# Performance work log

Hardware: AMD Instinct MI355X
Metric: run time of the kernel (lower is better)

Reference implementation:

```python
import jax, jax.numpy as jnp
import numpy as np

NODE_SIZE = 50000
REL_SIZE = 2000
TRIPLE_SIZE = 1000000
HID = 128
DEPTH = 2


def _rows_covering(key, n_rows, n_seg):
    # sorted row indices guaranteeing every segment appears at least once
    extra = jax.random.randint(key, (n_rows - n_seg,), 0, n_seg)
    return jnp.sort(jnp.concatenate([jnp.arange(n_seg), extra])).astype(jnp.int32)


def setup_inputs() -> dict:
    key = jax.random.key(0)
    ks = jax.random.split(key, 12)
    adj = jnp.stack([_rows_covering(ks[0], TRIPLE_SIZE, NODE_SIZE),
                     jax.random.randint(ks[1], (TRIPLE_SIZE,), 0, NODE_SIZE, dtype=jnp.int32)])
    r_index = jnp.stack([jnp.arange(TRIPLE_SIZE, dtype=jnp.int32),
                         jax.random.randint(ks[2], (TRIPLE_SIZE,), 0, REL_SIZE, dtype=jnp.int32)])
    r_val = jax.random.uniform(ks[3], (TRIPLE_SIZE,), dtype=jnp.float32)
    ent_adj = jnp.stack([_rows_covering(ks[4], TRIPLE_SIZE, NODE_SIZE),
                         jax.random.randint(ks[5], (TRIPLE_SIZE,), 0, NODE_SIZE, dtype=jnp.int32)])
    rel_adj = jnp.stack([_rows_covering(ks[6], TRIPLE_SIZE, NODE_SIZE),
                         jax.random.randint(ks[7], (TRIPLE_SIZE,), 0, REL_SIZE, dtype=jnp.int32)])
    ent_emb = jax.random.normal(ks[8], (NODE_SIZE, HID), dtype=jnp.float32) * 0.05
    rel_emb = jax.random.normal(ks[9], (REL_SIZE, HID), dtype=jnp.float32) * 0.05
    attn_e = jax.random.normal(ks[10], (DEPTH, HID, 1), dtype=jnp.float32) * 0.1
    attn_r = jax.random.normal(ks[11], (DEPTH, HID, 1), dtype=jnp.float32) * 0.1
    return {"ent_emb": ent_emb, "rel_emb": rel_emb, "attn_e": attn_e, "attn_r": attn_r,
            "adj": adj, "r_index": r_index, "r_val": r_val,
            "ent_adj": ent_adj, "rel_adj": rel_adj}


def _avg(adj, emb, node_size):
    # sparse softmax over all-ones values == mean over neighbors
    rows, cols = adj[0], adj[1]
    deg = jax.ops.segment_sum(jnp.ones_like(rows, dtype=emb.dtype), rows, node_size)
    s = jax.ops.segment_sum(emb[cols], rows, node_size)  # [node_size, d]
    return s / jnp.maximum(deg, 1.0)[:, None]


def _segment_softmax(vals, seg, num_seg):
    m = jax.ops.segment_max(vals, seg, num_seg)
    e = jnp.exp(vals - m[seg])
    s = jax.ops.segment_sum(e, seg, num_seg)
    return e / s[seg]


def _nr_graph_attention(features, rel_emb, adj, r_index, r_val, attn_kernels):
    feats = jnp.tanh(features)
    outs = [feats]
    src, dst = adj[0], adj[1]
    for l in range(DEPTH):
        # sparse [T, R] @ rel_emb -> per-triple relation vector
        tri_rel = jax.ops.segment_sum(r_val[:, None] * rel_emb[r_index[1]], r_index[0], TRIPLE_SIZE)
        tri_rel = tri_rel / jnp.maximum(jnp.linalg.norm(tri_rel, axis=1, keepdims=True), 1e-12)
        neighs = feats[dst]  # [T, H]
        # Householder reflection of neighbor feature about tri_rel
        neighs = neighs - 2.0 * jnp.sum(neighs * tri_rel, axis=1, keepdims=True) * tri_rel
        att = jnp.squeeze(tri_rel @ attn_kernels[l], axis=-1)  # [T]
        a = _segment_softmax(att, src, NODE_SIZE)
        feats = jnp.tanh(jax.ops.segment_sum(neighs * a[:, None], src, NODE_SIZE))
        outs.append(feats)
    return jnp.concatenate(outs, axis=-1)  # [N, H*(DEPTH+1)]


def reference(ent_emb, rel_emb, attn_e, attn_r, adj, r_index, r_val, ent_adj, rel_adj):
    ent_feature = _avg(ent_adj, ent_emb, NODE_SIZE)  # [N, H]
    rel_feature = _avg(rel_adj, rel_emb, NODE_SIZE)  # [N, H]
    out_rel = _nr_graph_attention(rel_feature, rel_emb, adj, r_index, r_val, attn_r)
    out_ent = _nr_graph_attention(ent_feature, rel_emb, adj, r_index, r_val, attn_e)
    return jnp.concatenate([out_ent, out_rel], axis=-1)  # dropout rate 0 -> identity
```

## Files before the change

### kernel.cpp

```cpp
#include <hip/hip_runtime.h>
#include <hip/hip_fp16.h>
#include <math.h>

#define NN 50000
#define NR 2000
#define NT 1000000
#define HID 128
#define OSTRIDE 768
#define CH 256

typedef float f32x4 __attribute__((ext_vector_type(4)));
typedef unsigned u32x4 __attribute__((ext_vector_type(4)));
typedef unsigned u32x2 __attribute__((ext_vector_type(2)));
typedef _Float16 h16x2 __attribute__((ext_vector_type(2)));
typedef _Float16 h16x8 __attribute__((ext_vector_type(8)));

union U4H8 { u32x4 u; h16x8 h; };

__device__ __forceinline__ float wsum64(float v) {
#pragma unroll
  for (int off = 32; off > 0; off >>= 1) v += __shfl_xor(v, off, 64);
  return v;
}
__device__ __forceinline__ unsigned pack2(float x, float y) {
  __half2 h = __floats2half2_rn(x, y);
  union { __half2 h; unsigned u; } c; c.h = h; return c.u;
}
__device__ __forceinline__ float2 unpack2(unsigned u) {
  union { unsigned u; __half2 h; } c; c.u = u;
  return __half22float2(c.h);
}
__device__ __forceinline__ void nt_store4(const float4& v, float* p) {
  f32x4 t = {v.x, v.y, v.z, v.w};
  __builtin_nontemporal_store(t, (f32x4*)p);
}

__global__ void rowptr3_kernel(const int* __restrict__ a0, int* __restrict__ r0,
                               const int* __restrict__ a1, int* __restrict__ r1,
                               const int* __restrict__ a2, int* __restrict__ r2) {
  const int* rows = (blockIdx.y == 0) ? a0 : (blockIdx.y == 1) ? a1 : a2;
  int* rp = (blockIdx.y == 0) ? r0 : (blockIdx.y == 1) ? r1 : r2;
  int i = blockIdx.x * blockDim.x + threadIdx.x;
  int stride = gridDim.x * blockDim.x;
  for (int t = i; t < NT; t += stride) {
    if (t == 0 || rows[t] != rows[t - 1]) rp[rows[t]] = t;
  }
  if (i == 0) rp[NN] = NT;
}

__global__ __launch_bounds__(256) void relpre_kernel(
    const float* __restrict__ rel_emb, const float* __restrict__ attn_e,
    const float* __restrict__ attn_r, float4* __restrict__ e4,
    float* __restrict__ n2i_arr) {
  int wid = (blockIdx.x * blockDim.x + threadIdx.x) >> 6;
  int lane = threadIdx.x & 63;
  if (wid >= NR) return;
  const float2* e2 = (const float2*)rel_emb;
  float2 e = e2[(size_t)wid * 64 + lane];
  float p = wsum64(e.x * e.x + e.y * e.y);
  float inv_n = rsqrtf(p);
  const float* ks[4] = {attn_e, attn_e + HID, attn_r, attn_r + HID};
  float d[4];
#pragma unroll
  for (int j = 0; j < 4; ++j) {
    float2 a = ((const float2*)ks[j])[lane];
    d[j] = wsum64(e.x * a.x + e.y * a.y);
  }
  if (lane == 0) {
    e4[wid] = make_float4(expf(d[0] * inv_n), expf(d[1] * inv_n),
                          expf(d[2] * inv_n), expf(d[3] * inv_n));
    n2i_arr[wid] = 1.f / p;
  }
}

__global__ __launch_bounds__(256) void cvt_kernel(const float* __restrict__ ent,
                                                  const float* __restrict__ rel,
                                                  __half* __restrict__ enth,
                                                  __half* __restrict__ relh) {
  int i = blockIdx.x * blockDim.x + threadIdx.x;
  const int entu = NN * 16;
  const float4* s4;
  u32x4* d;
  int j;
  if (i < entu) {
    s4 = (const float4*)ent; d = (u32x4*)enth; j = i;
  } else {
    j = i - entu;
    if (j >= NR * 16) return;
    s4 = (const float4*)rel; d = (u32x4*)relh;
  }
  float4 a = s4[2 * j], b = s4[2 * j + 1];
  u32x4 w;
  w.x = pack2(a.x, a.y); w.y = pack2(a.z, a.w);
  w.z = pack2(b.x, b.y); w.w = pack2(b.z, b.w);
  __builtin_nontemporal_store(w, d + j);
}

__global__ __launch_bounds__(256) void wpre2_kernel(
    const int* __restrict__ rp, const int* __restrict__ dst,
    const int* __restrict__ rel_id, const float* __restrict__ r_val,
    const float4* __restrict__ e4, const float* __restrict__ n2i_arr,
    unsigned* __restrict__ pk, u32x2* __restrict__ wq0,
    u32x2* __restrict__ wq1) {
  int wid = (blockIdx.x * blockDim.x + threadIdx.x) >> 6;
  int lane = threadIdx.x & 63;
  if (wid >= NN) return;
  int t0 = rp[wid], t1 = rp[wid + 1];
  float4 s = make_float4(0.f, 0.f, 0.f, 0.f);
  for (int t = t0 + lane; t < t1; t += 64) {
    int r = rel_id[t];
    float rv = r_val[t];
    float4 ex = e4[r];
    if (rv <= 0.f) ex = make_float4(1.f, 1.f, 1.f, 1.f);
    s.x += ex.x; s.y += ex.y; s.z += ex.z; s.w += ex.w;
  }
  s.x = wsum64(s.x); s.y = wsum64(s.y); s.z = wsum64(s.z); s.w = wsum64(s.w);
  float4 inv = make_float4(1.f / s.x, 1.f / s.y, 1.f / s.z, 1.f / s.w);
  for (int t = t0 + lane; t < t1; t += 64) {
    int r = rel_id[t];
    float rv = r_val[t];
    int dn = dst[t];
    float4 ex = e4[r];
    float zi = n2i_arr[r];
    if (rv <= 0.f) { ex = make_float4(1.f, 1.f, 1.f, 1.f); zi = 0.f; }
    float we0 = ex.x * inv.x, wr0 = ex.z * inv.z;
    float we1 = ex.y * inv.y, wr1 = ex.w * inv.w;
    __builtin_nontemporal_store((unsigned)dn | ((unsigned)r << 16), pk + t);
    u32x2 a, b;
    a.x = pack2(we0, wr0); a.y = pack2(-2.f * we0 * zi, -2.f * wr0 * zi);
    b.x = pack2(we1, wr1); b.y = pack2(-2.f * we1 * zi, -2.f * wr1 * zi);
    __builtin_nontemporal_store(a, wq0 + t);
    __builtin_nontemporal_store(b, wq1 + t);
  }
}

__global__ __launch_bounds__(256) void avg_tanh_kernel(
    const int* __restrict__ rp_ent, const int* __restrict__ cols_ent,
    const int* __restrict__ rp_rel, const int* __restrict__ cols_rel,
    const __half* __restrict__ enth, const __half* __restrict__ relh,
    float* __restrict__ out, __half* __restrict__ c0h) {
  int wid = (blockIdx.x * blockDim.x + threadIdx.x) >> 6;
  int lane = threadIdx.x & 63;
  if (wid >= NN) return;
  int br = (wid >= NN / 2) ? 1 : 0;
  int pair = wid - br * (NN / 2);
  int node = pair * 2 + (lane >> 5);
  int sl = lane & 31;
  const int* rp = br ? rp_rel : rp_ent;
  const int* cols = br ? cols_rel : cols_ent;
  const u32x2* eb = (const u32x2*)(br ? relh : enth);
  int t0 = rp[node], t1 = rp[node + 1];
  int nmax = t1 - 1;

  int c0 = cols[t0];
  int c1 = cols[min(t0 + 1, nmax)];
  int c2 = cols[min(t0 + 2, nmax)];
  int c3 = cols[min(t0 + 3, nmax)];
  u32x2 h0 = eb[(size_t)c0 * 32 + sl];
  u32x2 h1 = eb[(size_t)c1 * 32 + sl];
  u32x2 h2 = eb[(size_t)c2 * 32 + sl];
  u32x2 h3 = eb[(size_t)c3 * 32 + sl];
  int d0 = cols[min(t0 + 4, nmax)];
  int d1 = cols[min(t0 + 5, nmax)];
  int d2 = cols[min(t0 + 6, nmax)];
  int d3 = cols[min(t0 + 7, nmax)];

  float4 acc = make_float4(0.f, 0.f, 0.f, 0.f);
  for (int t = t0; t < t1; t += 4) {
    u32x2 g0 = eb[(size_t)d0 * 32 + sl];
    u32x2 g1 = eb[(size_t)d1 * 32 + sl];
    u32x2 g2 = eb[(size_t)d2 * 32 + sl];
    u32x2 g3 = eb[(size_t)d3 * 32 + sl];
    int tm = t + 8;
    int n0 = cols[min(tm, nmax)];
    int n1 = cols[min(tm + 1, nmax)];
    int n2 = cols[min(tm + 2, nmax)];
    int n3 = cols[min(tm + 3, nmax)];
    float m1 = (t + 1 < t1) ? 1.f : 0.f;
    float m2 = (t + 2 < t1) ? 1.f : 0.f;
    float m3 = (t + 3 < t1) ? 1.f : 0.f;
    float2 a0 = unpack2(h0.x), b0v = unpack2(h0.y);
    float2 a1 = unpack2(h1.x), b1v = unpack2(h1.y);
    float2 a2 = unpack2(h2.x), b2v = unpack2(h2.y);
    float2 a3 = unpack2(h3.x), b3v = unpack2(h3.y);
    acc.x += a0.x + m1 * a1.x + m2 * a2.x + m3 * a3.x;
    acc.y += a0.y + m1 * a1.y + m2 * a2.y + m3 * a3.y;
    acc.z += b0v.x + m1 * b1v.x + m2 * b2v.x + m3 * b3v.x;
    acc.w += b0v.y + m1 * b1v.y + m2 * b2v.y + m3 * b3v.y;
    h0 = g0; h1 = g1; h2 = g2; h3 = g3;
    d0 = n0; d1 = n1; d2 = n2; d3 = n3;
  }
  float inv = 1.f / (float)(t1 - t0);
  float4 o;
  o.x = tanhf(acc.x * inv); o.y = tanhf(acc.y * inv);
  o.z = tanhf(acc.z * inv); o.w = tanhf(acc.w * inv);
  nt_store4(o, out + (size_t)node * OSTRIDE + (br ? 3 * HID : 0) + sl * 4);
  u32x2 w; w.x = pack2(o.x, o.y); w.y = pack2(o.z, o.w);
  __builtin_nontemporal_store(w, (u32x2*)(c0h + (size_t)node * CH + br * HID + sl * 4));
}

struct RecT { int dn; int r; float we, wr, ce, cr; };

__device__ __forceinline__ RecT ldrec(int t, int t1,
                                      const unsigned* __restrict__ pk,
                                      const u32x2* __restrict__ wq) {
  bool valid = (t < t1);
  int tc = valid ? t : (t1 - 1);
  unsigned p = pk[tc];
  u32x2 w = wq[tc];
  RecT rec;
  rec.dn = (int)(p & 0xFFFFu);
  rec.r = (int)(p >> 16);
  float2 a = unpack2(w.x);
  float2 b = unpack2(w.y);
  rec.we = valid ? a.x : 0.f;
  rec.wr = valid ? a.y : 0.f;
  rec.ce = valid ? b.x : 0.f;
  rec.cr = valid ? b.y : 0.f;
  return rec;
}

__global__ __launch_bounds__(256) void attn_kernel(
    float* __restrict__ out, const int* __restrict__ rp,
    const unsigned* __restrict__ pk, const u32x2* __restrict__ wq,
    const __half* __restrict__ relh, const __half* __restrict__ chin,
    __half* __restrict__ chout, int layer) {
  int wid = (blockIdx.x * blockDim.x + threadIdx.x) >> 6;
  int lane = threadIdx.x & 63;
  if (wid >= NN) return;
  int g = lane >> 4;
  int sl = lane & 15;
  int t0 = rp[wid], t1 = rp[wid + 1];

  const u32x4* relh4 = (const u32x4*)relh;
  RecT b0 = ldrec(t0 + g, t1, pk, wq);
  float aE[8], aR[8];
#pragma unroll
  for (int i = 0; i < 8; ++i) { aE[i] = 0.f; aR[i] = 0.f; }

  for (int tb = t0; tb < t1; tb += 4) {
    U4H8 uh, eh, qh;
    uh.u = relh4[(size_t)b0.r * 16 + sl];
    const u32x4* ph = (const u32x4*)chin + (size_t)b0.dn * 32;
    eh.u = ph[sl];
    qh.u = ph[16 + sl];
    RecT b1 = ldrec(tb + 4 + g, t1, pk, wq);

    float de = 0.f, dr = 0.f;
#if __has_builtin(__builtin_amdgcn_fdot2)
#pragma unroll
    for (int i = 0; i < 4; ++i) {
      h16x2 up = {uh.h[2 * i], uh.h[2 * i + 1]};
      h16x2 ep = {eh.h[2 * i], eh.h[2 * i + 1]};
      h16x2 qp = {qh.h[2 * i], qh.h[2 * i + 1]};
      de = __builtin_amdgcn_fdot2(up, ep, de, false);
      dr = __builtin_amdgcn_fdot2(up, qp, dr, false);
    }
#else
#pragma unroll
    for (int i = 0; i < 8; ++i) {
      de += (float)uh.h[i] * (float)eh.h[i];
      dr += (float)uh.h[i] * (float)qh.h[i];
    }
#endif
#pragma unroll
    for (int off = 1; off < 16; off <<= 1) {
      de += __shfl_xor(de, off, 64);
      dr += __shfl_xor(dr, off, 64);
    }
    float ce = b0.ce * de;
    float cr = b0.cr * dr;
#pragma unroll
    for (int i = 0; i < 8; ++i) {
      float uf = (float)uh.h[i];
      aE[i] += b0.we * (float)eh.h[i] + ce * uf;
      aR[i] += b0.wr * (float)qh.h[i] + cr * uf;
    }
    b0 = b1;
  }

#pragma unroll
  for (int i = 0; i < 8; ++i) {
    aE[i] += __shfl_xor(aE[i], 16, 64);
    aE[i] += __shfl_xor(aE[i], 32, 64);
    aR[i] += __shfl_xor(aR[i], 16, 64);
    aR[i] += __shfl_xor(aR[i], 32, 64);
  }

  float4 v;
  if (g == 0) v = make_float4(aE[0], aE[1], aE[2], aE[3]);
  else if (g == 1) v = make_float4(aE[4], aE[5], aE[6], aE[7]);
  else if (g == 2) v = make_float4(aR[0], aR[1], aR[2], aR[3]);
  else v = make_float4(aR[4], aR[5], aR[6], aR[7]);
  v.x = tanhf(v.x); v.y = tanhf(v.y); v.z = tanhf(v.z); v.w = tanhf(v.w);
  float* ob = (g < 2) ? (out + (size_t)wid * OSTRIDE + (layer + 1) * HID)
                      : (out + (size_t)wid * OSTRIDE + (4 + layer) * HID);
  nt_store4(v, ob + sl * 8 + (g & 1) * 4);
  if (chout) {
    u32x2 w; w.x = pack2(v.x, v.y); w.y = pack2(v.z, v.w);
    __builtin_nontemporal_store(
        w, (u32x2*)(chout + (size_t)wid * CH + (g >> 1) * 128 + sl * 8 + (g & 1) * 4));
  }
}

extern "C" void kernel_launch(void* const* d_in, const int* in_sizes, int n_in,
                              void* d_out, int out_size, void* d_ws, size_t ws_size,
                              hipStream_t stream) {
  const float* ent_emb = (const float*)d_in[0];
  const float* rel_emb = (const float*)d_in[1];
  const float* attn_e = (const float*)d_in[2];
  const float* attn_r = (const float*)d_in[3];
  const int* adj = (const int*)d_in[4];
  const int* r_index = (const int*)d_in[5];
  const float* r_val = (const float*)d_in[6];
  const int* ent_adj = (const int*)d_in[7];
  const int* rel_adj = (const int*)d_in[8];
  float* out = (float*)d_out;

  char* ws = (char*)d_ws;
  __half* enth = (__half*)ws;  ws += (size_t)NN * HID * sizeof(__half);
  __half* relh = (__half*)ws;  ws += (size_t)NR * HID * sizeof(__half);
  __half* C0h = (__half*)ws;   ws += (size_t)NN * CH * sizeof(__half);
  __half* C1h = (__half*)ws;   ws += (size_t)NN * CH * sizeof(__half);
  unsigned* pk = (unsigned*)ws; ws += (size_t)NT * sizeof(unsigned);
  u32x2* wq0 = (u32x2*)ws;     ws += (size_t)NT * sizeof(u32x2);
  u32x2* wq1 = (u32x2*)ws;     ws += (size_t)NT * sizeof(u32x2);
  float4* e4 = (float4*)ws;    ws += (size_t)NR * sizeof(float4);
  float* n2i = (float*)ws;     ws += (size_t)NR * sizeof(float);
  int* rp_adj = (int*)ws;      ws += (NN + 1) * sizeof(int);
  int* rp_ent = (int*)ws;      ws += (NN + 1) * sizeof(int);
  int* rp_rel = (int*)ws;      ws += (NN + 1) * sizeof(int);

  dim3 rg(512, 3);
  rowptr3_kernel<<<rg, 256, 0, stream>>>(adj, rp_adj, ent_adj, rp_ent, rel_adj, rp_rel);
  relpre_kernel<<<(NR * 64) / 256, 256, 0, stream>>>(rel_emb, attn_e, attn_r, e4, n2i);
  cvt_kernel<<<((NN + NR) * 16) / 256, 256, 0, stream>>>(ent_emb, rel_emb, enth, relh);
  wpre2_kernel<<<(NN * 64) / 256, 256, 0, stream>>>(
      rp_adj, adj + NT, r_index + NT, r_val, e4, n2i, pk, wq0, wq1);
  avg_tanh_kernel<<<(NN * 64) / 256, 256, 0, stream>>>(
      rp_ent, ent_adj + NT, rp_rel, rel_adj + NT, enth, relh, out, C0h);
  for (int l = 0; l < 2; ++l) {
    attn_kernel<<<(NN * 64) / 256, 256, 0, stream>>>(
        out, rp_adj, pk, (l == 0) ? wq0 : wq1, relh,
        (l == 0) ? C0h : C1h, (l == 0) ? C1h : nullptr, l);
  }
}
```

Before: 468.5 us.

## Fuse prep kernels, merge averaging with weight precompute, unroll gather loops

Merges the relation precompute and fp16 conversion into one launch, and merges the neighbor-averaging kernel with the attention-weight precompute as independent block ranges of one grid. The weight precompute now uses 16 lanes per node instead of a full wavefront per node. The averaging loop gathers 8 neighbors per iteration with select-masking, and the attention loop processes two edge records per iteration. The goal is fewer launches, less idle lane work on short rows, and more memory-level parallelism, at the cost of more registers per thread.

```diff
diff --git a/kernel.cpp b/kernel.cpp
--- a/kernel.cpp
+++ b/kernel.cpp
@@ -48,46 +48,43 @@
   if (i == 0) rp[NN] = NT;
 }
 
-__global__ __launch_bounds__(256) void relpre_kernel(
+__global__ __launch_bounds__(256) void prep_kernel(
     const float* __restrict__ rel_emb, const float* __restrict__ attn_e,
     const float* __restrict__ attn_r, float4* __restrict__ e4,
-    float* __restrict__ n2i_arr) {
+    float* __restrict__ n2i_arr, const float* __restrict__ ent_emb,
+    __half* __restrict__ enth, __half* __restrict__ relh) {
   int wid = (blockIdx.x * blockDim.x + threadIdx.x) >> 6;
   int lane = threadIdx.x & 63;
-  if (wid >= NR) return;
-  const float2* e2 = (const float2*)rel_emb;
-  float2 e = e2[(size_t)wid * 64 + lane];
-  float p = wsum64(e.x * e.x + e.y * e.y);
-  float inv_n = rsqrtf(p);
-  const float* ks[4] = {attn_e, attn_e + HID, attn_r, attn_r + HID};
-  float d[4];
-#pragma unroll
-  for (int j = 0; j < 4; ++j) {
-    float2 a = ((const float2*)ks[j])[lane];
-    d[j] = wsum64(e.x * a.x + e.y * a.y);
-  }
-  if (lane == 0) {
-    e4[wid] = make_float4(expf(d[0] * inv_n), expf(d[1] * inv_n),
-                          expf(d[2] * inv_n), expf(d[3] * inv_n));
-    n2i_arr[wid] = 1.f / p;
-  }
-}
-
-__global__ __launch_bounds__(256) void cvt_kernel(const float* __restrict__ ent,
-                                                  const float* __restrict__ rel,
-                                                  __half* __restrict__ enth,
-                                                  __half* __restrict__ relh) {
-  int i = blockIdx.x * blockDim.x + threadIdx.x;
+  if (wid < NR) {
+    const float2* e2 = (const float2*)rel_emb;
+    float2 e = e2[(size_t)wid * 64 + lane];
+    float p = wsum64(e.x * e.x + e.y * e.y);
+    float inv_n = rsqrtf(p);
+    const float* ks[4] = {attn_e, attn_e + HID, attn_r, attn_r + HID};
+    float d[4];
+#pragma unroll
+    for (int j = 0; j < 4; ++j) {
+      float2 a = ((const float2*)ks[j])[lane];
+      d[j] = wsum64(e.x * a.x + e.y * a.y);
+    }
+    if (lane == 0) {
+      e4[wid] = make_float4(expf(d[0] * inv_n), expf(d[1] * inv_n),
+                            expf(d[2] * inv_n), expf(d[3] * inv_n));
+      n2i_arr[wid] = 1.f / p;
+    }
+    return;
+  }
+  int i = (wid - NR) * 64 + lane;
   const int entu = NN * 16;
   const float4* s4;
   u32x4* d;
   int j;
   if (i < entu) {
-    s4 = (const float4*)ent; d = (u32x4*)enth; j = i;
+    s4 = (const float4*)ent_emb; d = (u32x4*)enth; j = i;
   } else {
     j = i - entu;
     if (j >= NR * 16) return;
-    s4 = (const float4*)rel; d = (u32x4*)relh;
+    s4 = (const float4*)rel_emb; d = (u32x4*)relh;
   }
   float4 a = s4[2 * j], b = s4[2 * j + 1];
   u32x4 w;
@@ -96,27 +93,111 @@
   __builtin_nontemporal_store(w, d + j);
 }
 
-__global__ __launch_bounds__(256) void wpre2_kernel(
-    const int* __restrict__ rp, const int* __restrict__ dst,
+__global__ __launch_bounds__(256) void avgwpre_kernel(
+    const int* __restrict__ rp_ent, const int* __restrict__ cols_ent,
+    const int* __restrict__ rp_rel, const int* __restrict__ cols_rel,
+    const __half* __restrict__ enth, const __half* __restrict__ relh,
+    float* __restrict__ out, __half* __restrict__ c0h,
+    const int* __restrict__ rp_adj, const int* __restrict__ dst,
     const int* __restrict__ rel_id, const float* __restrict__ r_val,
     const float4* __restrict__ e4, const float* __restrict__ n2i_arr,
     unsigned* __restrict__ pk, u32x2* __restrict__ wq0,
     u32x2* __restrict__ wq1) {
   int wid = (blockIdx.x * blockDim.x + threadIdx.x) >> 6;
   int lane = threadIdx.x & 63;
-  if (wid >= NN) return;
-  int t0 = rp[wid], t1 = rp[wid + 1];
-  float4 s = make_float4(0.f, 0.f, 0.f, 0.f);
-  for (int t = t0 + lane; t < t1; t += 64) {
+
+  if (wid < NN) {
+    int br = (wid >= NN / 2) ? 1 : 0;
+    int pair = wid - br * (NN / 2);
+    int node = pair * 2 + (lane >> 5);
+    int sl = lane & 31;
+    const int* rp = br ? rp_rel : rp_ent;
+    const int* cols = br ? cols_rel : cols_ent;
+    const u32x2* eb = (const u32x2*)(br ? relh : enth);
+    int t0 = rp[node], t1 = rp[node + 1];
+    int nmax = t1 - 1;
+    int i0 = cols[t0];
+    int i1 = cols[min(t0 + 1, nmax)];
+    int i2 = cols[min(t0 + 2, nmax)];
+    int i3 = cols[min(t0 + 3, nmax)];
+    int i4 = cols[min(t0 + 4, nmax)];
+    int i5 = cols[min(t0 + 5, nmax)];
+    int i6 = cols[min(t0 + 6, nmax)];
+    int i7 = cols[min(t0 + 7, nmax)];
+    float4 acc = make_float4(0.f, 0.f, 0.f, 0.f);
+    const u32x2 z = {0u, 0u};
+    for (int t = t0; t < t1; t += 8) {
+      u32x2 h0 = eb[(size_t)i0 * 32 + sl];
+      u32x2 h1 = eb[(size_t)i1 * 32 + sl];
+      u32x2 h2 = eb[(size_t)i2 * 32 + sl];
+      u32x2 h3 = eb[(size_t)i3 * 32 + sl];
+      u32x2 h4 = eb[(size_t)i4 * 32 + sl];
+      u32x2 h5 = eb[(size_t)i5 * 32 + sl];
+      u32x2 h6 = eb[(size_t)i6 * 32 + sl];
+      u32x2 h7 = eb[(size_t)i7 * 32 + sl];
+      int tn = t + 8;
+      i0 = cols[min(tn, nmax)];
+      i1 = cols[min(tn + 1, nmax)];
+      i2 = cols[min(tn + 2, nmax)];
+      i3 = cols[min(tn + 3, nmax)];
+      i4 = cols[min(tn + 4, nmax)];
+      i5 = cols[min(tn + 5, nmax)];
+      i6 = cols[min(tn + 6, nmax)];
+      i7 = cols[min(tn + 7, nmax)];
+      h1 = (t + 1 < t1) ? h1 : z;
+      h2 = (t + 2 < t1) ? h2 : z;
+      h3 = (t + 3 < t1) ? h3 : z;
+      h4 = (t + 4 < t1) ? h4 : z;
+      h5 = (t + 5 < t1) ? h5 : z;
+      h6 = (t + 6 < t1) ? h6 : z;
+      h7 = (t + 7 < t1) ? h7 : z;
+      float2 a0 = unpack2(h0.x), b0 = unpack2(h0.y);
+      float2 a1 = unpack2(h1.x), b1 = unpack2(h1.y);
+      float2 a2 = unpack2(h2.x), b2 = unpack2(h2.y);
+      float2 a3 = unpack2(h3.x), b3 = unpack2(h3.y);
+      float2 a4 = unpack2(h4.x), b4 = unpack2(h4.y);
+      float2 a5 = unpack2(h5.x), b5 = unpack2(h5.y);
+      float2 a6 = unpack2(h6.x), b6 = unpack2(h6.y);
+      float2 a7 = unpack2(h7.x), b7 = unpack2(h7.y);
+      acc.x += ((a0.x + a1.x) + (a2.x + a3.x)) + ((a4.x + a5.x) + (a6.x + a7.x));
+      acc.y += ((a0.y + a1.y) + (a2.y + a3.y)) + ((a4.y + a5.y) + (a6.y + a7.y));
+      acc.z += ((b0.x + b1.x) + (b2.x + b3.x)) + ((b4.x + b5.x) + (b6.x + b7.x));
+      acc.w += ((b0.y + b1.y) + (b2.y + b3.y)) + ((b4.y + b5.y) + (b6.y + b7.y));
+    }
+    float inv = 1.f / (float)(t1 - t0);
+    float4 o;
+    o.x = tanhf(acc.x * inv); o.y = tanhf(acc.y * inv);
+    o.z = tanhf(acc.z * inv); o.w = tanhf(acc.w * inv);
+    nt_store4(o, out + (size_t)node * OSTRIDE + (br ? 3 * HID : 0) + sl * 4);
+    u32x2 w; w.x = pack2(o.x, o.y); w.y = pack2(o.z, o.w);
+    __builtin_nontemporal_store(w,
+        (u32x2*)(c0h + (size_t)node * CH + br * HID + sl * 4));
+    return;
+  }
+
+  wid -= NN;
+  if (wid >= NN / 4) return;
+  int sub = lane >> 4;
+  int s = lane & 15;
+  int node = wid * 4 + sub;
+  int t0 = rp_adj[node], t1 = rp_adj[node + 1];
+  float4 ss = make_float4(0.f, 0.f, 0.f, 0.f);
+  for (int t = t0 + s; t < t1; t += 16) {
     int r = rel_id[t];
     float rv = r_val[t];
     float4 ex = e4[r];
     if (rv <= 0.f) ex = make_float4(1.f, 1.f, 1.f, 1.f);
-    s.x += ex.x; s.y += ex.y; s.z += ex.z; s.w += ex.w;
-  }
-  s.x = wsum64(s.x); s.y = wsum64(s.y); s.z = wsum64(s.z); s.w = wsum64(s.w);
-  float4 inv = make_float4(1.f / s.x, 1.f / s.y, 1.f / s.z, 1.f / s.w);
-  for (int t = t0 + lane; t < t1; t += 64) {
+    ss.x += ex.x; ss.y += ex.y; ss.z += ex.z; ss.w += ex.w;
+  }
+#pragma unroll
+  for (int off = 1; off < 16; off <<= 1) {
+    ss.x += __shfl_xor(ss.x, off, 64);
+    ss.y += __shfl_xor(ss.y, off, 64);
+    ss.z += __shfl_xor(ss.z, off, 64);
+    ss.w += __shfl_xor(ss.w, off, 64);
+  }
+  float4 inv = make_float4(1.f / ss.x, 1.f / ss.y, 1.f / ss.z, 1.f / ss.w);
+  for (int t = t0 + s; t < t1; t += 16) {
     int r = rel_id[t];
     float rv = r_val[t];
     int dn = dst[t];
@@ -132,71 +213,6 @@
     __builtin_nontemporal_store(a, wq0 + t);
     __builtin_nontemporal_store(b, wq1 + t);
   }
-}
-
-__global__ __launch_bounds__(256) void avg_tanh_kernel(
-    const int* __restrict__ rp_ent, const int* __restrict__ cols_ent,
-    const int* __restrict__ rp_rel, const int* __restrict__ cols_rel,
-    const __half* __restrict__ enth, const __half* __restrict__ relh,
-    float* __restrict__ out, __half* __restrict__ c0h) {
-  int wid = (blockIdx.x * blockDim.x + threadIdx.x) >> 6;
-  int lane = threadIdx.x & 63;
-  if (wid >= NN) return;
-  int br = (wid >= NN / 2) ? 1 : 0;
-  int pair = wid - br * (NN / 2);
-  int node = pair * 2 + (lane >> 5);
-  int sl = lane & 31;
-  const int* rp = br ? rp_rel : rp_ent;
-  const int* cols = br ? cols_rel : cols_ent;
-  const u32x2* eb = (const u32x2*)(br ? relh : enth);
-  int t0 = rp[node], t1 = rp[node + 1];
-  int nmax = t1 - 1;
-
-  int c0 = cols[t0];
-  int c1 = cols[min(t0 + 1, nmax)];
-  int c2 = cols[min(t0 + 2, nmax)];
-  int c3 = cols[min(t0 + 3, nmax)];
-  u32x2 h0 = eb[(size_t)c0 * 32 + sl];
-  u32x2 h1 = eb[(size_t)c1 * 32 + sl];
-  u32x2 h2 = eb[(size_t)c2 * 32 + sl];
-  u32x2 h3 = eb[(size_t)c3 * 32 + sl];
-  int d0 = cols[min(t0 + 4, nmax)];
-  int d1 = cols[min(t0 + 5, nmax)];
-  int d2 = cols[min(t0 + 6, nmax)];
-  int d3 = cols[min(t0 + 7, nmax)];
-
-  float4 acc = make_float4(0.f, 0.f, 0.f, 0.f);
-  for (int t = t0; t < t1; t += 4) {
-    u32x2 g0 = eb[(size_t)d0 * 32 + sl];
-    u32x2 g1 = eb[(size_t)d1 * 32 + sl];
-    u32x2 g2 = eb[(size_t)d2 * 32 + sl];
-    u32x2 g3 = eb[(size_t)d3 * 32 + sl];
-    int tm = t + 8;
-    int n0 = cols[min(tm, nmax)];
-    int n1 = cols[min(tm + 1, nmax)];
-    int n2 = cols[min(tm + 2, nmax)];
-    int n3 = cols[min(tm + 3, nmax)];
-    float m1 = (t + 1 < t1) ? 1.f : 0.f;
-    float m2 = (t + 2 < t1) ? 1.f : 0.f;
-    float m3 = (t + 3 < t1) ? 1.f : 0.f;
-    float2 a0 = unpack2(h0.x), b0v = unpack2(h0.y);
-    float2 a1 = unpack2(h1.x), b1v = unpack2(h1.y);
-    float2 a2 = unpack2(h2.x), b2v = unpack2(h2.y);
-    float2 a3 = unpack2(h3.x), b3v = unpack2(h3.y);
-    acc.x += a0.x + m1 * a1.x + m2 * a2.x + m3 * a3.x;
-    acc.y += a0.y + m1 * a1.y + m2 * a2.y + m3 * a3.y;
-    acc.z += b0v.x + m1 * b1v.x + m2 * b2v.x + m3 * b3v.x;
-    acc.w += b0v.y + m1 * b1v.y + m2 * b2v.y + m3 * b3v.y;
-    h0 = g0; h1 = g1; h2 = g2; h3 = g3;
-    d0 = n0; d1 = n1; d2 = n2; d3 = n3;
-  }
-  float inv = 1.f / (float)(t1 - t0);
-  float4 o;
-  o.x = tanhf(acc.x * inv); o.y = tanhf(acc.y * inv);
-  o.z = tanhf(acc.z * inv); o.w = tanhf(acc.w * inv);
-  nt_store4(o, out + (size_t)node * OSTRIDE + (br ? 3 * HID : 0) + sl * 4);
-  u32x2 w; w.x = pack2(o.x, o.y); w.y = pack2(o.z, o.w);
-  __builtin_nontemporal_store(w, (u32x2*)(c0h + (size_t)node * CH + br * HID + sl * 4));
 }
 
 struct RecT { int dn; int r; float we, wr, ce, cr; };
@@ -233,50 +249,71 @@
   int t0 = rp[wid], t1 = rp[wid + 1];
 
   const u32x4* relh4 = (const u32x4*)relh;
-  RecT b0 = ldrec(t0 + g, t1, pk, wq);
+  RecT A = ldrec(t0 + g, t1, pk, wq);
+  RecT B = ldrec(t0 + 4 + g, t1, pk, wq);
   float aE[8], aR[8];
 #pragma unroll
   for (int i = 0; i < 8; ++i) { aE[i] = 0.f; aR[i] = 0.f; }
 
-  for (int tb = t0; tb < t1; tb += 4) {
-    U4H8 uh, eh, qh;
-    uh.u = relh4[(size_t)b0.r * 16 + sl];
-    const u32x4* ph = (const u32x4*)chin + (size_t)b0.dn * 32;
-    eh.u = ph[sl];
-    qh.u = ph[16 + sl];
-    RecT b1 = ldrec(tb + 4 + g, t1, pk, wq);
-
-    float de = 0.f, dr = 0.f;
+  for (int tb = t0; tb < t1; tb += 8) {
+    U4H8 uhA, ehA, qhA, uhB, ehB, qhB;
+    uhA.u = relh4[(size_t)A.r * 16 + sl];
+    const u32x4* phA = (const u32x4*)chin + (size_t)A.dn * 32;
+    ehA.u = phA[sl];
+    qhA.u = phA[16 + sl];
+    uhB.u = relh4[(size_t)B.r * 16 + sl];
+    const u32x4* phB = (const u32x4*)chin + (size_t)B.dn * 32;
+    ehB.u = phB[sl];
+    qhB.u = phB[16 + sl];
+    RecT An = ldrec(tb + 8 + g, t1, pk, wq);
+    RecT Bn = ldrec(tb + 12 + g, t1, pk, wq);
+
+    float deA = 0.f, drA = 0.f, deB = 0.f, drB = 0.f;
 #if __has_builtin(__builtin_amdgcn_fdot2)
 #pragma unroll
     for (int i = 0; i < 4; ++i) {
-      h16x2 up = {uh.h[2 * i], uh.h[2 * i + 1]};
-      h16x2 ep = {eh.h[2 * i], eh.h[2 * i + 1]};
-      h16x2 qp = {qh.h[2 * i], qh.h[2 * i + 1]};
-      de = __builtin_amdgcn_fdot2(up, ep, de, false);
-      dr = __builtin_amdgcn_fdot2(up, qp, dr, false);
+      h16x2 uA = {uhA.h[2 * i], uhA.h[2 * i + 1]};
+      h16x2 eA = {ehA.h[2 * i], ehA.h[2 * i + 1]};
+      h16x2 qA = {qhA.h[2 * i], qhA.h[2 * i + 1]};
+      h16x2 uB = {uhB.h[2 * i], uhB.h[2 * i + 1]};
+      h16x2 eB = {ehB.h[2 * i], ehB.h[2 * i + 1]};
+      h16x2 qB = {qhB.h[2 * i], qhB.h[2 * i + 1]};
+      deA = __builtin_amdgcn_fdot2(uA, eA, deA, false);
+      drA = __builtin_amdgcn_fdot2(uA, qA, drA, false);
+      deB = __builtin_amdgcn_fdot2(uB, eB, deB, false);
+      drB = __builtin_amdgcn_fdot2(uB, qB, drB, false);
     }
 #else
 #pragma unroll
     for (int i = 0; i < 8; ++i) {
-      de += (float)uh.h[i] * (float)eh.h[i];
-      dr += (float)uh.h[i] * (float)qh.h[i];
+      deA += (float)uhA.h[i] * (float)ehA.h[i];
+      drA += (float)uhA.h[i] * (float)qhA.h[i];
+      deB += (float)uhB.h[i] * (float)ehB.h[i];
+      drB += (float)uhB.h[i] * (float)qhB.h[i];
     }
 #endif
 #pragma unroll
     for (int off = 1; off < 16; off <<= 1) {
-      de += __shfl_xor(de, off, 64);
-      dr += __shfl_xor(dr, off, 64);
-    }
-    float ce = b0.ce * de;
-    float cr = b0.cr * dr;
+      deA += __shfl_xor(deA, off, 64);
+      drA += __shfl_xor(drA, off, 64);
+      deB += __shfl_xor(deB, off, 64);
+      drB += __shfl_xor(drB, off, 64);
+    }
+    float ceA = A.ce * deA;
+    float crA = A.cr * drA;
+    float ceB = B.ce * deB;
+    float crB = B.cr * drB;
 #pragma unroll
     for (int i = 0; i < 8; ++i) {
-      float uf = (float)uh.h[i];
-      aE[i] += b0.we * (float)eh.h[i] + ce * uf;
-      aR[i] += b0.wr * (float)qh.h[i] + cr * uf;
-    }
-    b0 = b1;
+      float ufA = (float)uhA.h[i];
+      float ufB = (float)uhB.h[i];
+      aE[i] += A.we * (float)ehA.h[i] + ceA * ufA;
+      aE[i] += B.we * (float)ehB.h[i] + ceB * ufB;
+      aR[i] += A.wr * (float)qhA.h[i] + crA * ufA;
+      aR[i] += B.wr * (float)qhB.h[i] + crB * ufB;
+    }
+    A = An;
+    B = Bn;
   }
 
 #pragma unroll
@@ -333,12 +370,11 @@
 
   dim3 rg(512, 3);
   rowptr3_kernel<<<rg, 256, 0, stream>>>(adj, rp_adj, ent_adj, rp_ent, rel_adj, rp_rel);
-  relpre_kernel<<<(NR * 64) / 256, 256, 0, stream>>>(rel_emb, attn_e, attn_r, e4, n2i);
-  cvt_kernel<<<((NN + NR) * 16) / 256, 256, 0, stream>>>(ent_emb, rel_emb, enth, relh);
-  wpre2_kernel<<<(NN * 64) / 256, 256, 0, stream>>>(
+  prep_kernel<<<3750, 256, 0, stream>>>(rel_emb, attn_e, attn_r, e4, n2i,
+                                        ent_emb, enth, relh);
+  avgwpre_kernel<<<15625, 256, 0, stream>>>(
+      rp_ent, ent_adj + NT, rp_rel, rel_adj + NT, enth, relh, out, C0h,
       rp_adj, adj + NT, r_index + NT, r_val, e4, n2i, pk, wq0, wq1);
-  avg_tanh_kernel<<<(NN * 64) / 256, 256, 0, stream>>>(
-      rp_ent, ent_adj + NT, rp_rel, rel_adj + NT, enth, relh, out, C0h);
   for (int l = 0; l < 2; ++l) {
     attn_kernel<<<(NN * 64) / 256, 256, 0, stream>>>(
         out, rp_adj, pk, (l == 0) ? wq0 : wq1, relh,
```

Measured after the change: 467.7 us. Within noise of the previous version (-0.2%).
